# Optimization experiments

Measured on AMD Instinct MI355X. Metric: run time of the kernel, lower is better.

The kernel has to match this reference:

```python
import jax, jax.numpy as jnp
import numpy as np

IN_SIZE = 224
KERNEL = 5
STRIDE = 1
IN_CH = 16
OUT_CH = 64
LAMB = 5.0
LR = 0.005
GAMMA = 0.99
EPS_ = 0.01
NH = (IN_SIZE - KERNEL) // STRIDE + 1          # 220 output positions per side
NB_TILES = NH * NH                              # 48400 tiles


def setup_inputs() -> dict:
    key = jax.random.key(0)
    k1, k2 = jax.random.split(key)
    x = jax.random.normal(k1, (1, IN_CH, IN_SIZE, IN_SIZE), dtype=jnp.float32)
    # torch.nn.init.uniform_(param, a=0, b=1)
    W = jax.random.uniform(k2, (OUT_CH, IN_CH, KERNEL, KERNEL), dtype=jnp.float32)
    exp_avg = jnp.zeros((OUT_CH,), dtype=jnp.float32)
    return {"x": x, "W": W, "exp_avg": exp_avg, "clamped": 0}


def _inhibition(out):
    out = jax.nn.relu(out)
    m = jnp.max(out, axis=1, keepdims=True)     # max over channel dim
    out = out / (m + 1e-9)
    return out ** LAMB


def _flatten_input(x):
    # mirrors x.unfold(2,k,s).unfold(3,k,s) -> [T, C*k*k] with (C, kh, kw) ordering
    starts = jnp.arange(NH) * STRIDE
    rows = starts[:, None] + jnp.arange(KERNEL)  # [NH, K]
    p = x[0][:, rows]                            # [C, NH, K, W]
    p = p[:, :, :, rows]                         # [C, NH, K, NH, K]
    p = p.transpose(1, 3, 0, 2, 4)               # [NH, NH, C, K, K]
    return p.reshape(NB_TILES, -1)               # [T, D]


def reference(x, W, exp_avg, clamped):
    # forward conv + inhibition
    out = jax.lax.conv_general_dilated(
        x, W, (STRIDE, STRIDE), 'VALID',
        dimension_numbers=('NCHW', 'OIHW', 'NCHW'))
    out = _inhibition(out)                       # [1, O, NH, NH]

    # Hebbian FullyOrthogonal update (no-grad buffer update in the original)
    y = out[0].transpose(1, 2, 0).reshape(-1, OUT_CH)   # [T, O]
    xf = _flatten_input(x)                               # [T, D]
    Wf = W.reshape(OUT_CH, -1)                           # [O, D]
    # mean_t( lr * (y_t (x) x_t - y_t (x) (y_t W)) ) = lr/T * (Y^T X - (Y^T Y) W)
    yty = y.T @ y                                        # [O, O]
    avg_delta = (LR / NB_TILES) * (y.T @ xf - yty @ Wf)  # [O, D]
    Wnew = jax.nn.relu(Wf + avg_delta).reshape(OUT_CH, IN_CH, KERNEL, KERNEL)
    exp_new = GAMMA * exp_avg + (1.0 - GAMMA) * jnp.mean(y, axis=0)

    # weight decay scaling
    A = exp_new / jnp.mean(exp_new)
    gfp = EPS_ * jnp.tanh(-EPS_ * (A - 1.0)) + 1.0
    gfn = 1.0 / gfp
    pos = jnp.where(Wnew > 0, Wnew, 0.0) * gfp.reshape(-1, 1, 1, 1)
    neg = jnp.where(Wnew < 0, Wnew, 0.0) * gfn.reshape(-1, 1, 1, 1)
    Wfinal = pos + neg
    return out, Wfinal, exp_new
```

## Files before the change

kernel.cpp:

```cpp
#include <hip/hip_runtime.h>
#include <stdint.h>

#define IN_SIZE 224
#define KER 5
#define IN_CH 16
#define OUT_CH 64
#define NH 220
#define NB_TILES (NH * NH)
#define XCH (IN_SIZE * IN_SIZE)
#define OUT_PLANE NB_TILES
#define KP2 51200
#define XS 52224
#define XTROWS 50304
#define LR_OVER_NB ((float)(0.005 / 48400.0))
#define GAMMA_F 0.99f
#define ONE_MINUS_GAMMA 0.01f
#define EPS_F 0.01f

#define NCHUNK 64
#define CK 800
#define PSTRIDE (64 * 512)
#define BROW 24

typedef __attribute__((ext_vector_type(8))) short short8;
typedef __attribute__((ext_vector_type(4))) float floatx4;
typedef __attribute__((ext_vector_type(16))) float floatx16;

__device__ inline uint16_t f2bf(float f) {
    uint32_t u = __float_as_uint(f);
    return (uint16_t)((u + 0x7FFFu + ((u >> 16) & 1u)) >> 16);
}
__device__ inline float bf2f(uint16_t h) { return __uint_as_float((uint32_t)h << 16); }

__global__ __launch_bounds__(256) void prepa_kernel(const float* __restrict__ x,
                                                    uint16_t* __restrict__ xth,
                                                    uint16_t* __restrict__ xtl,
                                                    const float* __restrict__ W,
                                                    uint16_t* __restrict__ wrh,
                                                    uint16_t* __restrict__ wrl) {
    int blk = blockIdx.x;
    if (blk < 197) {
        int addr = blk * 256 + threadIdx.x;
        if (addr >= XTROWS) return;
        uint32_t dh[8], dl[8];
        if (addr < XCH) {
#pragma unroll
            for (int q = 0; q < 8; q++) {
                float v0 = x[(2 * q) * XCH + addr];
                float v1 = x[(2 * q + 1) * XCH + addr];
                uint16_t h0 = f2bf(v0), h1 = f2bf(v1);
                uint16_t l0 = f2bf(v0 - bf2f(h0)), l1 = f2bf(v1 - bf2f(h1));
                dh[q] = (uint32_t)h0 | ((uint32_t)h1 << 16);
                dl[q] = (uint32_t)l0 | ((uint32_t)l1 << 16);
            }
        } else {
#pragma unroll
            for (int q = 0; q < 8; q++) { dh[q] = 0u; dl[q] = 0u; }
        }
        *(uint4*)(xth + addr * 16) = make_uint4(dh[0], dh[1], dh[2], dh[3]);
        *(uint4*)(xth + addr * 16 + 8) = make_uint4(dh[4], dh[5], dh[6], dh[7]);
        *(uint4*)(xtl + addr * 16) = make_uint4(dl[0], dl[1], dl[2], dl[3]);
        *(uint4*)(xtl + addr * 16 + 8) = make_uint4(dl[4], dl[5], dl[6], dl[7]);
    } else {
        int idx = (blk - 197) * 256 + threadIdx.x;
        if (idx >= 25600) return;
        int j = idx & 7;
        int lane = (idx >> 3) & 63;
        int ocg = (idx >> 9) & 1;
        int tap = idx >> 10;
        int oc = ocg * 32 + (lane & 31);
        int c = ((lane >> 5) << 3) + j;
        float v = W[oc * 400 + c * 25 + tap];
        uint16_t h = f2bf(v);
        wrh[idx] = h;
        wrl[idx] = f2bf(v - bf2f(h));
    }
}

__global__ __launch_bounds__(256) void conv_prep_kernel(const uint16_t* __restrict__ xth,
                                                        const uint16_t* __restrict__ xtl,
                                                        const uint16_t* __restrict__ wrh,
                                                        const uint16_t* __restrict__ wrl,
                                                        float* __restrict__ out,
                                                        uint16_t* __restrict__ yb,
                                                        const float* __restrict__ x,
                                                        uint16_t* __restrict__ xs,
                                                        uint16_t* __restrict__ ones) {
    if (blockIdx.x >= 770) {
        int t = (blockIdx.x - 770) * 256 + threadIdx.x;
        const int perq = XS / 4;
        if (t < 5 * 16 * perq) {
            int kj = t / (16 * perq);
            int rem = t - kj * (16 * perq);
            int c = rem / perq;
            int q = (rem - c * perq) * 4;
            int base = c * XCH;
            ushort4 o;
            int i0 = q + kj;     o.x = f2bf(x[base + (i0 < XCH ? i0 : XCH - 1)]);
            int i1 = q + kj + 1; o.y = f2bf(x[base + (i1 < XCH ? i1 : XCH - 1)]);
            int i2 = q + kj + 2; o.z = f2bf(x[base + (i2 < XCH ? i2 : XCH - 1)]);
            int i3 = q + kj + 3; o.w = f2bf(x[base + (i3 < XCH ? i3 : XCH - 1)]);
            *(ushort4*)(xs + (kj * 16 + c) * XS + q) = o;
        }
        ushort4 z = {0, 0, 0, 0};
        if (t < 64 * 480) {
            int r = t / 480, q = (t - r * 480) * 4;
            *(ushort4*)(yb + r * KP2 + 49280 + q) = z;
        }
        if (t < 64 * 220) {
            int o = t / 220, i = t - o * 220;
            *(ushort4*)(yb + o * KP2 + i * 224 + 220) = z;
        }
        if (t < 12816) {
            ushort4 o1 = {0x3F80, 0x3F80, 0x3F80, 0x3F80};
            ((ushort4*)ones)[t] = o1;
        }
        return;
    }

    const int lane = threadIdx.x & 63;
    const int w = threadIdx.x >> 6;
    const int ocg = w & 1;
    const int posg = w >> 1;
    const int l31 = lane & 31;
    const int kh = lane >> 5;
    const int c0 = kh * 8;
    const int P0 = blockIdx.x * 64;
    const int pl = posg * 32 + l31;

    __shared__ uint16_t bsh[5 * 68 * BROW];
    __shared__ uint16_t bsl[5 * 68 * BROW];
    for (int u = threadIdx.x; u < 680; u += 256) {
        int row = u >> 1;
        int half = (u & 1) * 8;
        int strip = row / 68;
        int rr = row - strip * 68;
        int grow = P0 + strip * 224 + rr;
        *(uint4*)(bsh + row * BROW + half) = *(const uint4*)(xth + grow * 16 + half);
        *(uint4*)(bsl + row * BROW + half) = *(const uint4*)(xtl + grow * 16 + half);
    }
    __syncthreads();

    floatx16 acc = {0.f, 0.f, 0.f, 0.f, 0.f, 0.f, 0.f, 0.f,
                    0.f, 0.f, 0.f, 0.f, 0.f, 0.f, 0.f, 0.f};

#pragma unroll
    for (int t = 0; t < 25; t++) {
        short8 ah = *(const short8*)(wrh + ((t * 2 + ocg) * 64 + lane) * 8);
        short8 al = *(const short8*)(wrl + ((t * 2 + ocg) * 64 + lane) * 8);
        const int ki = t / 5, kj = t % 5;
        const int lrow = ki * 68 + pl + kj;
        short8 bh = *(const short8*)(bsh + lrow * BROW + c0);
        short8 bl = *(const short8*)(bsl + lrow * BROW + c0);
        acc = __builtin_amdgcn_mfma_f32_32x32x16_bf16(ah, bh, acc, 0, 0, 0);
        acc = __builtin_amdgcn_mfma_f32_32x32x16_bf16(ah, bl, acc, 0, 0, 0);
        acc = __builtin_amdgcn_mfma_f32_32x32x16_bf16(al, bh, acc, 0, 0, 0);
    }

    float mx = 0.f;
#pragma unroll
    for (int r = 0; r < 16; r++) mx = fmaxf(mx, acc[r]);
    mx = fmaxf(mx, 0.f);
    mx = fmaxf(mx, __shfl_xor(mx, 32));

    __shared__ float wmax2[2][64];
    if (lane < 32) wmax2[ocg][pl] = mx;
    __syncthreads();
    float mall = fmaxf(wmax2[0][pl], wmax2[1][pl]);
    float inv = 1.f / (mall + 1e-9f);

    int P = P0 + pl;
    int i = P / 224;
    int j = P - i * 224;
    bool valid = j < NH;
#pragma unroll
    for (int r = 0; r < 16; r++) {
        int oc = ocg * 32 + (r & 3) + 8 * (r >> 2) + 4 * kh;
        float tv = fmaxf(acc[r], 0.f) * inv;
        float t2 = tv * tv;
        tv = t2 * t2 * tv;
        if (valid) {
            out[oc * OUT_PLANE + i * NH + j] = tv;
            yb[oc * KP2 + P] = f2bf(tv);
        }
    }
}

__global__ __launch_bounds__(256) void gemm_kernel(const uint16_t* __restrict__ yb,
                                                   const uint16_t* __restrict__ xs,
                                                   const uint16_t* __restrict__ ones,
                                                   uint16_t* __restrict__ Mpart) {
    __shared__ uint16_t As[2][64 * 40];
    __shared__ uint16_t Bs[2][64 * 40];
    const int tid = threadIdx.x;
    const int lane = tid & 63;
    const int w = tid >> 6;
    const int l15 = lane & 15;
    const int quad = lane >> 4;
    const int kg = quad * 8;
    const int b = blockIdx.x;
    const int xcd = b & 7;
    const int t8 = b >> 3;
    const int ntile = t8 & 7;
    const int chunk = xcd + 8 * (t8 >> 3);
    const int k0 = chunk * CK;

    const int sr = tid >> 2;
    const int sseg = (tid & 3) * 8;
    const uint16_t* pa = yb + sr * KP2 + k0 + sseg;

    int n_g = ntile * 64 + sr;
    const uint16_t* pbase;
    if (n_g < 400) {
        int c = n_g / 25;
        int r = n_g - 25 * c;
        int ki = r / 5;
        int kj = r - 5 * ki;
        pbase = xs + (kj * 16 + c) * XS + ki * 224;
    } else if (n_g < 464) {
        pbase = yb + (n_g - 400) * KP2;
    } else if (n_g == 464) {
        pbase = ones;
    } else {
        pbase = yb;
    }
    const uint16_t* pb = pbase + k0 + sseg;

    floatx4 acc[4];
#pragma unroll
    for (int i = 0; i < 4; i++) acc[i] = (floatx4){0.f, 0.f, 0.f, 0.f};

    uint4 ra = *(const uint4*)pa;
    uint4 rb = *(const uint4*)pb;

    for (int s = 0; s < 25; s++) {
        const int p = s & 1;
        *(uint4*)&As[p][sr * 40 + sseg] = ra;
        *(uint4*)&Bs[p][sr * 40 + sseg] = rb;
        __syncthreads();
        if (s + 1 < 25) {
            pa += 32;
            pb += 32;
            ra = *(const uint4*)pa;
            rb = *(const uint4*)pb;
        }
        short8 af = *(const short8*)&As[p][(16 * w + l15) * 40 + kg];
#pragma unroll
        for (int ng = 0; ng < 4; ng++) {
            short8 bf = *(const short8*)&Bs[p][(16 * ng + l15) * 40 + kg];
            acc[ng] = __builtin_amdgcn_mfma_f32_16x16x32_bf16(af, bf, acc[ng], 0, 0, 0);
        }
    }

    uint16_t* dst = Mpart + chunk * PSTRIDE;
#pragma unroll
    for (int ng = 0; ng < 4; ng++) {
        int col = ntile * 64 + ng * 16 + l15;
        if (col < 465) {
#pragma unroll
            for (int r = 0; r < 4; r++)
                dst[(16 * w + quad * 4 + r) * 512 + col] = f2bf(acc[ng][r]);
        }
    }
}

__global__ __launch_bounds__(256) void finalize_w_kernel(const float* __restrict__ W,
                                                         const uint16_t* __restrict__ Mpart,
                                                         const float* __restrict__ exp_avg,
                                                         float* __restrict__ Wout,
                                                         float* __restrict__ expout) {
    __shared__ float gfps[OUT_CH];
    __shared__ float ytys[2][OUT_CH];
    const int tid = threadIdx.x;
    const int bid = blockIdx.x;
    const int first_o = (bid * 256) / 400;

    if (tid < OUT_CH) {
        int o = tid;
        float cs = 0.f;
#pragma unroll 8
        for (int ch = 0; ch < NCHUNK; ch++) cs += bf2f(Mpart[ch * PSTRIDE + o * 512 + 464]);
        float e = GAMMA_F * exp_avg[o] + ONE_MINUS_GAMMA * (cs / (float)NB_TILES);
        float s = e;
        for (int off = 32; off; off >>= 1) s += __shfl_down(s, off);
        s = __shfl(s, 0);
        float A = e / (s / (float)OUT_CH);
        gfps[o] = EPS_F * tanhf(-EPS_F * (A - 1.f)) + 1.f;
        if (bid == 0) expout[o] = e;
    }
    if (tid >= 128) {
        int t = tid - 128;
        int orow = first_o + (t >> 6);
        int k = t & 63;
        float s = 0.f;
        if (orow < OUT_CH) {
#pragma unroll 8
            for (int ch = 0; ch < NCHUNK; ch++) s += bf2f(Mpart[ch * PSTRIDE + orow * 512 + 400 + k]);
        }
        ytys[t >> 6][k] = s;
    }
    __syncthreads();

    int idx = bid * 256 + tid;
    int o = idx / 400;
    int q = idx - o * 400;
    float Mv = 0.f;
#pragma unroll 8
    for (int ch = 0; ch < NCHUNK; ch++) Mv += bf2f(Mpart[ch * PSTRIDE + o * 512 + q]);
    const float* yrow = ytys[o - first_o];
    float dot = 0.f;
#pragma unroll 8
    for (int k = 0; k < OUT_CH; k++) dot = fmaf(yrow[k], W[k * 400 + q], dot);
    float wv = W[idx] + LR_OVER_NB * (Mv - dot);
    wv = fmaxf(wv, 0.f);
    float gp = gfps[o];
    float pos = (wv > 0.f ? wv : 0.f) * gp;
    float neg = (wv < 0.f ? wv : 0.f) / gp;
    Wout[idx] = pos + neg;
}

extern "C" void kernel_launch(void* const* d_in, const int* in_sizes, int n_in,
                              void* d_out, int out_size, void* d_ws, size_t ws_size,
                              hipStream_t stream) {
    const float* x = (const float*)d_in[0];
    const float* W = (const float*)d_in[1];
    const float* exp_avg = (const float*)d_in[2];
    float* out = (float*)d_out;

    uint16_t* base = (uint16_t*)d_ws;
    uint16_t* Mpart = base;
    uint16_t* xth = base;
    uint16_t* xtl = xth + XTROWS * 16;
    uint16_t* wrh = xtl + XTROWS * 16;
    uint16_t* wrl = wrh + 25600;
    uint16_t* ybf = base + NCHUNK * PSTRIDE;
    uint16_t* xsb = ybf + OUT_CH * KP2;
    uint16_t* ones = xsb + 5 * 16 * XS;

    float* Wout = out + OUT_CH * OUT_PLANE;
    float* expout = Wout + OUT_CH * IN_CH * KER * KER;

    prepa_kernel<<<297, 256, 0, stream>>>(x, xth, xtl, W, wrh, wrl);
    conv_prep_kernel<<<770 + 4080, 256, 0, stream>>>(xth, xtl, wrh, wrl, out, ybf, x, xsb, ones);
    gemm_kernel<<<512, 256, 0, stream>>>(ybf, xsb, ones, Mpart);
    finalize_w_kernel<<<100, 256, 0, stream>>>(W, Mpart, exp_avg, Wout, expout);
}
```

Baseline: 110.2 us.

## Double conv tile per block and rebalance GEMM K-split into more chunks

The conv kernel now computes 128 positions per block with two accumulators per wave, so each weight fragment load feeds twice as many MFMAs and the block count halves. The shared staging row stride changes from 24 to 16 elements, which removes padding and may raise LDS bank conflicts. Separately, the GEMM splits K into 80 chunks of 640 instead of 64 of 800, launching 640 blocks to improve occupancy at the cost of more partial sums for finalize to reduce. Finalize must already handle NCHUNK generically and PSTRIDE must fit 80 chunks, which the hidden code cannot confirm.

Measured after the change: 113.2 us. 2.7% more time.

```diff
diff --git a/kernel.cpp b/kernel.cpp
--- a/kernel.cpp
+++ b/kernel.cpp
@@ -17,10 +17,10 @@
 #define ONE_MINUS_GAMMA 0.01f
 #define EPS_F 0.01f
 
-#define NCHUNK 64
-#define CK 800
+#define NCHUNK 80
+#define CK 640
 #define PSTRIDE (64 * 512)
-#define BROW 24
+#define CONVB 385
 
 typedef __attribute__((ext_vector_type(8))) short short8;
 typedef __attribute__((ext_vector_type(4))) float floatx4;
@@ -86,8 +86,8 @@
                                                         const float* __restrict__ x,
                                                         uint16_t* __restrict__ xs,
                                                         uint16_t* __restrict__ ones) {
-    if (blockIdx.x >= 770) {
-        int t = (blockIdx.x - 770) * 256 + threadIdx.x;
+    if (blockIdx.x >= CONVB) {
+        int t = (blockIdx.x - CONVB) * 256 + threadIdx.x;
         const int perq = XS / 4;
         if (t < 5 * 16 * perq) {
             int kj = t / (16 * perq);
@@ -125,63 +125,75 @@
     const int l31 = lane & 31;
     const int kh = lane >> 5;
     const int c0 = kh * 8;
-    const int P0 = blockIdx.x * 64;
-    const int pl = posg * 32 + l31;
-
-    __shared__ uint16_t bsh[5 * 68 * BROW];
-    __shared__ uint16_t bsl[5 * 68 * BROW];
-    for (int u = threadIdx.x; u < 680; u += 256) {
+    const int P0 = blockIdx.x * 128;
+
+    __shared__ uint16_t bsh[5 * 132 * 16];
+    __shared__ uint16_t bsl[5 * 132 * 16];
+    for (int u = threadIdx.x; u < 1320; u += 256) {
         int row = u >> 1;
         int half = (u & 1) * 8;
-        int strip = row / 68;
-        int rr = row - strip * 68;
+        int strip = row / 132;
+        int rr = row - strip * 132;
         int grow = P0 + strip * 224 + rr;
-        *(uint4*)(bsh + row * BROW + half) = *(const uint4*)(xth + grow * 16 + half);
-        *(uint4*)(bsl + row * BROW + half) = *(const uint4*)(xtl + grow * 16 + half);
+        *(uint4*)(bsh + row * 16 + half) = *(const uint4*)(xth + grow * 16 + half);
+        *(uint4*)(bsl + row * 16 + half) = *(const uint4*)(xtl + grow * 16 + half);
     }
     __syncthreads();
 
-    floatx16 acc = {0.f, 0.f, 0.f, 0.f, 0.f, 0.f, 0.f, 0.f,
-                    0.f, 0.f, 0.f, 0.f, 0.f, 0.f, 0.f, 0.f};
+    floatx16 acc0 = {0.f, 0.f, 0.f, 0.f, 0.f, 0.f, 0.f, 0.f,
+                     0.f, 0.f, 0.f, 0.f, 0.f, 0.f, 0.f, 0.f};
+    floatx16 acc1 = acc0;
 
 #pragma unroll
     for (int t = 0; t < 25; t++) {
         short8 ah = *(const short8*)(wrh + ((t * 2 + ocg) * 64 + lane) * 8);
         short8 al = *(const short8*)(wrl + ((t * 2 + ocg) * 64 + lane) * 8);
         const int ki = t / 5, kj = t % 5;
-        const int lrow = ki * 68 + pl + kj;
-        short8 bh = *(const short8*)(bsh + lrow * BROW + c0);
-        short8 bl = *(const short8*)(bsl + lrow * BROW + c0);
-        acc = __builtin_amdgcn_mfma_f32_32x32x16_bf16(ah, bh, acc, 0, 0, 0);
-        acc = __builtin_amdgcn_mfma_f32_32x32x16_bf16(ah, bl, acc, 0, 0, 0);
-        acc = __builtin_amdgcn_mfma_f32_32x32x16_bf16(al, bh, acc, 0, 0, 0);
-    }
-
-    float mx = 0.f;
-#pragma unroll
-    for (int r = 0; r < 16; r++) mx = fmaxf(mx, acc[r]);
-    mx = fmaxf(mx, 0.f);
-    mx = fmaxf(mx, __shfl_xor(mx, 32));
-
-    __shared__ float wmax2[2][64];
-    if (lane < 32) wmax2[ocg][pl] = mx;
+        const int lbase = ki * 132 + posg * 64 + l31 + kj;
+        short8 bh0 = *(const short8*)(bsh + lbase * 16 + c0);
+        short8 bl0 = *(const short8*)(bsl + lbase * 16 + c0);
+        short8 bh1 = *(const short8*)(bsh + (lbase + 32) * 16 + c0);
+        short8 bl1 = *(const short8*)(bsl + (lbase + 32) * 16 + c0);
+        acc0 = __builtin_amdgcn_mfma_f32_32x32x16_bf16(ah, bh0, acc0, 0, 0, 0);
+        acc0 = __builtin_amdgcn_mfma_f32_32x32x16_bf16(ah, bl0, acc0, 0, 0, 0);
+        acc0 = __builtin_amdgcn_mfma_f32_32x32x16_bf16(al, bh0, acc0, 0, 0, 0);
+        acc1 = __builtin_amdgcn_mfma_f32_32x32x16_bf16(ah, bh1, acc1, 0, 0, 0);
+        acc1 = __builtin_amdgcn_mfma_f32_32x32x16_bf16(ah, bl1, acc1, 0, 0, 0);
+        acc1 = __builtin_amdgcn_mfma_f32_32x32x16_bf16(al, bh1, acc1, 0, 0, 0);
+    }
+
+    __shared__ float wmax2[2][128];
+    float mx0 = 0.f, mx1 = 0.f;
+#pragma unroll
+    for (int r = 0; r < 16; r++) { mx0 = fmaxf(mx0, acc0[r]); mx1 = fmaxf(mx1, acc1[r]); }
+    mx0 = fmaxf(fmaxf(mx0, 0.f), __shfl_xor(fmaxf(mx0, 0.f), 32));
+    mx1 = fmaxf(fmaxf(mx1, 0.f), __shfl_xor(fmaxf(mx1, 0.f), 32));
+    if (lane < 32) {
+        wmax2[ocg][posg * 64 + l31] = mx0;
+        wmax2[ocg][posg * 64 + 32 + l31] = mx1;
+    }
     __syncthreads();
-    float mall = fmaxf(wmax2[0][pl], wmax2[1][pl]);
-    float inv = 1.f / (mall + 1e-9f);
-
-    int P = P0 + pl;
-    int i = P / 224;
-    int j = P - i * 224;
-    bool valid = j < NH;
-#pragma unroll
-    for (int r = 0; r < 16; r++) {
-        int oc = ocg * 32 + (r & 3) + 8 * (r >> 2) + 4 * kh;
-        float tv = fmaxf(acc[r], 0.f) * inv;
-        float t2 = tv * tv;
-        tv = t2 * t2 * tv;
-        if (valid) {
-            out[oc * OUT_PLANE + i * NH + j] = tv;
-            yb[oc * KP2 + P] = f2bf(tv);
+
+#pragma unroll
+    for (int sub = 0; sub < 2; sub++) {
+        int pin = posg * 64 + sub * 32 + l31;
+        float mall = fmaxf(wmax2[0][pin], wmax2[1][pin]);
+        float inv = 1.f / (mall + 1e-9f);
+        int P = P0 + pin;
+        int i = P / 224;
+        int j = P - i * 224;
+        bool valid = j < NH;
+        floatx16 a = sub ? acc1 : acc0;
+#pragma unroll
+        for (int r = 0; r < 16; r++) {
+            int oc = ocg * 32 + (r & 3) + 8 * (r >> 2) + 4 * kh;
+            float tv = fmaxf(a[r], 0.f) * inv;
+            float t2 = tv * tv;
+            tv = t2 * t2 * tv;
+            if (valid) {
+                out[oc * OUT_PLANE + i * NH + j] = tv;
+                yb[oc * KP2 + P] = f2bf(tv);
+            }
         }
     }
 }
@@ -233,12 +245,12 @@
     uint4 ra = *(const uint4*)pa;
     uint4 rb = *(const uint4*)pb;
 
-    for (int s = 0; s < 25; s++) {
+    for (int s = 0; s < 20; s++) {
         const int p = s & 1;
         *(uint4*)&As[p][sr * 40 + sseg] = ra;
         *(uint4*)&Bs[p][sr * 40 + sseg] = rb;
         __syncthreads();
-        if (s + 1 < 25) {
+        if (s + 1 < 20) {
             pa += 32;
             pb += 32;
             ra = *(const uint4*)pa;
@@ -341,7 +353,7 @@
     float* expout = Wout + OUT_CH * IN_CH * KER * KER;
 
     prepa_kernel<<<297, 256, 0, stream>>>(x, xth, xtl, W, wrh, wrl);
-    conv_prep_kernel<<<770 + 4080, 256, 0, stream>>>(xth, xtl, wrh, wrl, out, ybf, x, xsb, ones);
-    gemm_kernel<<<512, 256, 0, stream>>>(ybf, xsb, ones, Mpart);
+    conv_prep_kernel<<<CONVB + 4080, 256, 0, stream>>>(xth, xtl, wrh, wrl, out, ybf, x, xsb, ones);
+    gemm_kernel<<<640, 256, 0, stream>>>(ybf, xsb, ones, Mpart);
     finalize_w_kernel<<<100, 256, 0, stream>>>(W, Mpart, exp_avg, Wout, expout);
 }
```
